# Kernel optimization log

Measured on AMD Instinct MI355X. Metric: run time of the kernel, lower is better.

Reference implementation:

```python
import jax, jax.numpy as jnp
import numpy as np

N = 177          # hardcoded in update(): view(1, 177, out_channels)
HEADS = 1
OUT = 128
EDGE_DIM = 1
NEG_SLOPE = 0.2
E = 500000


def _glorot(key, shape):
    stdv = np.sqrt(6.0 / (shape[-2] + shape[-1])).astype(np.float32)
    return jax.random.uniform(key, shape, jnp.float32, -stdv, stdv)


def setup_inputs() -> dict:
    key = jax.random.key(0)
    ks = jax.random.split(key, 6)
    x = jax.random.normal(ks[0], (1, N, 128), jnp.float32)
    edge_index = jax.random.randint(ks[1], (2, E), 0, N)
    edge_attr = jax.random.normal(ks[2], (E, EDGE_DIM), jnp.float32)
    weight = _glorot(ks[3], (128, HEADS * OUT))
    att = _glorot(ks[4], (1, HEADS, 2 * OUT + EDGE_DIM))
    edge_update1 = _glorot(ks[5], (OUT + EDGE_DIM, OUT))
    bias = jnp.zeros((OUT,), jnp.float32)
    return {"x": x, "edge_attr": edge_attr, "weight": weight, "att": att,
            "edge_update1": edge_update1, "bias": bias, "edge_index": edge_index}


def reference(x, edge_attr, weight, att, edge_update1, bias, edge_index):
    # node transform: [N, in] @ [in, H*C] -> [N, H, C]
    h = (x[0] @ weight).reshape(-1, HEADS, OUT)
    src, dst = edge_index[0], edge_index[1]   # PyG: row 0 = source (j), row 1 = target (i)
    x_j = h[src]                              # [E, H, C]
    x_i = h[dst]                              # [E, H, C]
    ea = jnp.broadcast_to(edge_attr[:, None, :], (edge_attr.shape[0], HEADS, EDGE_DIM))
    x_j = jnp.concatenate([x_j, ea], axis=-1)              # [E, H, C+edge_dim]
    # attention logits: sum over feature axis of cat([x_i, x_j]) * att
    alpha = (jnp.concatenate([x_i, x_j], axis=-1) * att).sum(axis=-1)  # [E, H]
    alpha = jax.nn.leaky_relu(alpha, NEG_SLOPE)
    # scatter softmax over target nodes (two-pass: segment max then segment sum)
    amax = jax.ops.segment_max(alpha, dst, num_segments=N)             # [N, H]
    e = jnp.exp(alpha - amax[dst])
    esum = jax.ops.segment_sum(e, dst, num_segments=N)                 # [N, H]
    alpha = e / (esum[dst] + 1e-16)
    # weighted messages, scatter-add aggregation
    msg = x_j * alpha[:, :, None]                                      # [E, H, C+edge_dim]
    aggr = jax.ops.segment_sum(msg, dst, num_segments=N)               # [N, H, C+edge_dim]
    out = aggr.mean(axis=1) @ edge_update1 + bias                      # [N, C]
    return out.reshape(1, N, OUT)
```

## Files before the change

### kernel.cpp

```cpp
#include <hip/hip_runtime.h>

#define NN 177
#define NEG 0.2f
#define QR 45
#define ROWP 180
#define QSLOTS_P (QR * ROWP)
#define SL 8192
#define NCHUNK 64
#define EBLOCKS (NCHUNK * 4)
#define ETH 512

#define AIP_OFF  0
#define AJP_OFF  384
#define H_OFF    768
#define PART_OFF 23424

__device__ __forceinline__ float4 f4add(float4 a, float4 b) {
    return make_float4(a.x + b.x, a.y + b.y, a.z + b.z, a.w + b.w);
}

__global__ __launch_bounds__(256)
void k_nodeH(const float* __restrict__ x, const float* __restrict__ w,
             const float* __restrict__ att, float* __restrict__ ws) {
    const int n = blockIdx.x, half = blockIdx.y;
    const int tid = threadIdx.x;
    const int j = tid & 63, kq = tid >> 6;
    __shared__ float xl[128];
    __shared__ float ph[256];
    if (tid < 128) xl[tid] = x[n * 128 + tid];
    __syncthreads();
    const float* wp = w + (size_t)(kq * 32) * 128 + half * 64 + j;
    float acc = 0.f;
#pragma unroll 8
    for (int k = 0; k < 32; ++k) acc += xl[kq * 32 + k] * wp[(size_t)k * 128];
    ph[tid] = acc;
    __syncthreads();
    if (tid < 64) {
        float hv = ph[j] + ph[64 + j] + ph[128 + j] + ph[192 + j];
        ws[H_OFF + n * 128 + half * 64 + j] = hv;
        float pa = hv * att[half * 64 + j];
        float pb = hv * att[128 + half * 64 + j];
#pragma unroll
        for (int m = 1; m < 64; m <<= 1) {
            pa += __shfl_xor(pa, m);
            pb += __shfl_xor(pb, m);
        }
        if (j == 0) {
            ws[AIP_OFF + 2 * n + half] = pa;
            ws[AJP_OFF + 2 * n + half] = pb;
        }
    }
}

__global__ __launch_bounds__(ETH, 8)
void k_edge(const int* __restrict__ ei, const float* __restrict__ ea,
            const float* __restrict__ att, float* __restrict__ ws, int E, int CH) {
    const int chunk = blockIdx.x & (NCHUNK - 1), q = blockIdx.x >> 6;
    const int dlo = q * QR;
    int drows = NN - dlo; if (drows > QR) drows = QR;
    __shared__ __align__(16) float Wl[QSLOTS_P];
    __shared__ float ajl[NN], ailq[QR], Mq[QR], llast[QR], mred[64];
    int tid = threadIdx.x;
    const float4 z4 = make_float4(0.f, 0.f, 0.f, 0.f);
    for (int i = tid; i < QSLOTS_P / 4; i += ETH) ((float4*)Wl)[i] = z4;
    for (int i = tid; i < NN; i += ETH)
        ajl[i] = ws[AJP_OFF + 2 * i] + ws[AJP_OFF + 2 * i + 1];
    if (tid < QR) llast[tid] = 0.f;
    __syncthreads();
    if (tid < 64) {
        float m = -1e30f;
        for (int i = tid; i < NN; i += 64) m = fmaxf(m, ajl[i]);
        mred[tid] = m;
    }
    __syncthreads();
    if (tid < 16) mred[tid] = fmaxf(fmaxf(mred[tid], mred[tid + 16]),
                                    fmaxf(mred[tid + 32], mred[tid + 48]));
    __syncthreads();
    if (tid < 4) mred[tid] = fmaxf(fmaxf(mred[tid], mred[tid + 4]),
                                   fmaxf(mred[tid + 8], mred[tid + 12]));
    __syncthreads();
    if (tid == 0) mred[0] = fmaxf(fmaxf(mred[0], mred[1]), fmaxf(mred[2], mred[3]));
    __syncthreads();
    const float ajmax = mred[0];
    if (tid < drows) {
        float a = ws[AIP_OFF + 2 * (dlo + tid)] + ws[AIP_OFF + 2 * (dlo + tid) + 1];
        ailq[tid] = a;
        float M = a + ajmax + 1.0f;
        Mq[tid] = (M > 0.f) ? M : NEG * M;
    }
    const float cc = att[2 * 128];
    __syncthreads();

    const int base = chunk * CH;
    int lim = base + CH; if (lim > E) lim = E;
    const bool aligned4 = ((E & 3) == 0);
    for (int e0 = base + tid * 4; e0 < lim; e0 += ETH * 4) {
        int4 sv, dv; float4 eav;
        if (aligned4 && e0 + 3 < lim) {
            sv  = *(const int4*)(ei + e0);
            dv  = *(const int4*)(ei + E + e0);
            eav = *(const float4*)(ea + e0);
        } else {
            int e1 = lim - e0;
            sv.x = (e1 > 0) ? ei[e0]     : 0; dv.x = (e1 > 0) ? ei[E + e0]     : -1; eav.x = (e1 > 0) ? ea[e0]     : 0.f;
            sv.y = (e1 > 1) ? ei[e0 + 1] : 0; dv.y = (e1 > 1) ? ei[E + e0 + 1] : -1; eav.y = (e1 > 1) ? ea[e0 + 1] : 0.f;
            sv.z = (e1 > 2) ? ei[e0 + 2] : 0; dv.z = (e1 > 2) ? ei[E + e0 + 2] : -1; eav.z = (e1 > 2) ? ea[e0 + 2] : 0.f;
            sv.w = (e1 > 3) ? ei[e0 + 3] : 0; dv.w = (e1 > 3) ? ei[E + e0 + 3] : -1; eav.w = (e1 > 3) ? ea[e0 + 3] : 0.f;
        }
#define PROC(SS, DD, EE) do {                                   \
            int d_ = (DD) - dlo;                                \
            if ((unsigned)d_ < (unsigned)drows) {               \
                float t_ = ailq[d_] + ajl[SS] + cc * (EE);      \
                t_ = (t_ > 0.f) ? t_ : NEG * t_;                \
                float ev_ = __expf(t_ - Mq[d_]);                \
                atomicAdd(&Wl[d_ * ROWP + (SS)], ev_);          \
                atomicAdd(&llast[d_], ev_ * (EE));              \
            }                                                   \
        } while (0)
        PROC(sv.x, dv.x, eav.x);
        PROC(sv.y, dv.y, eav.y);
        PROC(sv.z, dv.z, eav.z);
        PROC(sv.w, dv.w, eav.w);
#undef PROC
    }
    __syncthreads();
    float* part = ws + PART_OFF + (size_t)blockIdx.x * SL;
    for (int i = tid; i < QSLOTS_P / 4; i += ETH)
        ((float4*)part)[i] = ((const float4*)Wl)[i];
    if (tid < QR) part[QSLOTS_P + tid] = llast[tid];
}

__global__ __launch_bounds__(ETH)
void k_outC(const float* __restrict__ ws, const float* __restrict__ eu,
            const float* __restrict__ bias, float* __restrict__ out) {
    __shared__ __align__(16) float wl[ROWP];
    __shared__ float vl[128];
    __shared__ float red[128];
    __shared__ float sc[2];
    __shared__ __align__(16) float hl[89 * 128];
    __shared__ __align__(16) float pd[2048];
    const int n = blockIdx.x, tid = threadIdx.x;
    const int q = n / QR, r = n % QR;
    const size_t qbase = PART_OFF + (size_t)q * NCHUNK * SL;

    {
        const int lane = tid & 63, cg = tid >> 6;
        const int s4 = lane * 4;
        float4 acc = make_float4(0.f, 0.f, 0.f, 0.f);
        if (s4 < ROWP) {
            const float* p = ws + qbase + (size_t)(cg * 8) * SL + (size_t)r * ROWP + s4;
#pragma unroll
            for (int ch = 0; ch < 8; ++ch)
                acc = f4add(acc, *(const float4*)(p + (size_t)ch * SL));
        }
        ((float4*)pd)[tid] = acc;
    }
    if (tid < 64) red[tid] = ws[qbase + (size_t)tid * SL + QSLOTS_P + r];
    __syncthreads();
    if (tid < 256) ((float4*)pd)[tid] = f4add(((float4*)pd)[tid], ((float4*)pd)[tid + 256]);
    if (tid < 32) red[tid] += red[tid + 32];
    __syncthreads();
    if (tid < 128) ((float4*)pd)[tid] = f4add(((float4*)pd)[tid], ((float4*)pd)[tid + 128]);
    if (tid < 16) red[tid] += red[tid + 16];
    __syncthreads();
    if (tid < 64) {
        float4 v = f4add(((float4*)pd)[tid], ((float4*)pd)[tid + 64]);
        if (tid * 4 < ROWP) ((float4*)wl)[tid] = v;
    }
    if (tid < 8) red[tid] += red[tid + 8];
    __syncthreads();
    if (tid == 0) {
        float wv = 0.f;
#pragma unroll
        for (int i = 0; i < 8; ++i) wv += red[i];
        sc[0] = wv;
    }
    __syncthreads();
    if (tid < 128) red[tid] = wl[tid] + ((tid + 128 < NN) ? wl[tid + 128] : 0.f);
    __syncthreads();
    for (int off = 64; off > 0; off >>= 1) {
        if (tid < off) red[tid] += red[tid + off];
        __syncthreads();
    }
    if (tid == 0) sc[1] = red[0];

    const int c = tid & 127, g = tid >> 7;
    float vacc = 0.f;
    __syncthreads();
    for (int i = tid; i < 89 * 32; i += ETH)
        ((float4*)hl)[i] = ((const float4*)(ws + H_OFF))[i];
    __syncthreads();
    {
        int s0 = (g * 89) >> 2, s1 = ((g + 1) * 89) >> 2;
        for (int s = s0; s < s1; ++s) vacc += wl[s] * hl[s * 128 + c];
    }
    __syncthreads();
    for (int i = tid; i < 88 * 32; i += ETH)
        ((float4*)hl)[i] = ((const float4*)(ws + H_OFF + 89 * 128))[i];
    __syncthreads();
    {
        int s0 = (g * 88) >> 2, s1 = ((g + 1) * 88) >> 2;
        for (int s = s0; s < s1; ++s) vacc += wl[89 + s] * hl[s * 128 + c];
    }
    pd[tid] = vacc;
    __syncthreads();
    if (tid < 128) vl[tid] = (pd[tid] + pd[128 + tid]) + (pd[256 + tid] + pd[384 + tid]);
    __syncthreads();

    {
        const int kg = tid >> 7;
        float oacc = 0.f;
        const float* ep = eu + (size_t)(kg * 32) * 128 + c;
#pragma unroll 8
        for (int k = 0; k < 32; ++k) oacc += vl[kg * 32 + k] * ep[(size_t)k * 128];
        pd[tid] = oacc;
    }
    __syncthreads();
    if (tid < 128) {
        float dot = (pd[tid] + pd[128 + tid]) + (pd[256 + tid] + pd[384 + tid]);
        out[n * 128 + tid] = (dot + sc[0] * eu[128 * 128 + tid]) / (sc[1] + 1e-16f) + bias[tid];
    }
}

extern "C" void kernel_launch(void* const* d_in, const int* in_sizes, int n_in,
                              void* d_out, int out_size, void* d_ws, size_t ws_size,
                              hipStream_t stream) {
    const float* x     = (const float*)d_in[0];
    const float* eattr = (const float*)d_in[1];
    const float* w     = (const float*)d_in[2];
    const float* att   = (const float*)d_in[3];
    const float* eu    = (const float*)d_in[4];
    const float* bias  = (const float*)d_in[5];
    const int*   ei    = (const int*)d_in[6];
    int E = in_sizes[6] / 2;
    int CH = (((E + NCHUNK - 1) / NCHUNK) + 3) & ~3;
    float* ws = (float*)d_ws;

    k_nodeH<<<dim3(NN, 2), 256, 0, stream>>>(x, w, att, ws);
    k_edge<<<EBLOCKS, ETH, 0, stream>>>(ei, eattr, att, ws, E, CH);
    k_outC<<<NN, ETH, 0, stream>>>(ws, eu, bias, (float*)d_out);
}
```

Baseline: 32.39 us.

## Fuse node transform into edge kernel via algebraic attention-vector precompute

Removes the separate node-transform kernel launch. Each edge block now computes u=W·att_i and v=W·att_j, then evaluates per-node attention logits as x·u and x·v redundantly for all nodes. The first 177 blocks also compute and store the full h rows needed by the output kernel. This saves a launch and the inter-kernel dependency, at the cost of redundant per-block prologue work (reading W and x in every block) and a slightly different floating-point summation order.

```diff
diff --git a/kernel.cpp b/kernel.cpp
--- a/kernel.cpp
+++ b/kernel.cpp
@@ -10,8 +10,6 @@
 #define EBLOCKS (NCHUNK * 4)
 #define ETH 512
 
-#define AIP_OFF  0
-#define AJP_OFF  384
 #define H_OFF    768
 #define PART_OFF 23424
 
@@ -19,54 +17,52 @@
     return make_float4(a.x + b.x, a.y + b.y, a.z + b.z, a.w + b.w);
 }
 
-__global__ __launch_bounds__(256)
-void k_nodeH(const float* __restrict__ x, const float* __restrict__ w,
-             const float* __restrict__ att, float* __restrict__ ws) {
-    const int n = blockIdx.x, half = blockIdx.y;
+__global__ __launch_bounds__(ETH)
+void k_edgeA(const float* __restrict__ x, const float* __restrict__ ea,
+             const float* __restrict__ w, const float* __restrict__ att,
+             const int* __restrict__ ei, float* __restrict__ ws, int E, int CH) {
+    __shared__ __align__(16) float Wl[QSLOTS_P];
+    __shared__ float ajl[NN], ail[NN], Mq[QR], llast[QR], mred[64];
+    __shared__ float uvec[128], vvec[128], atl[257], xl[128];
     const int tid = threadIdx.x;
-    const int j = tid & 63, kq = tid >> 6;
-    __shared__ float xl[128];
-    __shared__ float ph[256];
-    if (tid < 128) xl[tid] = x[n * 128 + tid];
-    __syncthreads();
-    const float* wp = w + (size_t)(kq * 32) * 128 + half * 64 + j;
-    float acc = 0.f;
-#pragma unroll 8
-    for (int k = 0; k < 32; ++k) acc += xl[kq * 32 + k] * wp[(size_t)k * 128];
-    ph[tid] = acc;
-    __syncthreads();
-    if (tid < 64) {
-        float hv = ph[j] + ph[64 + j] + ph[128 + j] + ph[192 + j];
-        ws[H_OFF + n * 128 + half * 64 + j] = hv;
-        float pa = hv * att[half * 64 + j];
-        float pb = hv * att[128 + half * 64 + j];
-#pragma unroll
-        for (int m = 1; m < 64; m <<= 1) {
-            pa += __shfl_xor(pa, m);
-            pb += __shfl_xor(pb, m);
-        }
-        if (j == 0) {
-            ws[AIP_OFF + 2 * n + half] = pa;
-            ws[AJP_OFF + 2 * n + half] = pb;
-        }
-    }
-}
-
-__global__ __launch_bounds__(ETH, 8)
-void k_edge(const int* __restrict__ ei, const float* __restrict__ ea,
-            const float* __restrict__ att, float* __restrict__ ws, int E, int CH) {
-    const int chunk = blockIdx.x & (NCHUNK - 1), q = blockIdx.x >> 6;
+    const int bid = blockIdx.x;
+    const int chunk = bid & (NCHUNK - 1), q = bid >> 6;
     const int dlo = q * QR;
     int drows = NN - dlo; if (drows > QR) drows = QR;
-    __shared__ __align__(16) float Wl[QSLOTS_P];
-    __shared__ float ajl[NN], ailq[QR], Mq[QR], llast[QR], mred[64];
-    int tid = threadIdx.x;
-    const float4 z4 = make_float4(0.f, 0.f, 0.f, 0.f);
-    for (int i = tid; i < QSLOTS_P / 4; i += ETH) ((float4*)Wl)[i] = z4;
-    for (int i = tid; i < NN; i += ETH)
-        ajl[i] = ws[AJP_OFF + 2 * i] + ws[AJP_OFF + 2 * i + 1];
-    if (tid < QR) llast[tid] = 0.f;
-    __syncthreads();
+
+    for (int i = tid; i < 257; i += ETH) atl[i] = att[i];
+    if (bid < NN && tid < 128) xl[tid] = x[bid * 128 + tid];
+    __syncthreads();
+
+    const float4* w4 = (const float4*)w;
+#pragma unroll
+    for (int i = 0; i < 8; ++i) {
+        int f = i * 512 + tid;
+        int k = f >> 5, c4 = (f & 31) << 2;
+        float4 wv = w4[f];
+        float pu = wv.x*atl[c4]     + wv.y*atl[c4+1]     + wv.z*atl[c4+2]     + wv.w*atl[c4+3];
+        float pv = wv.x*atl[128+c4] + wv.y*atl[128+c4+1] + wv.z*atl[128+c4+2] + wv.w*atl[128+c4+3];
+#pragma unroll
+        for (int m = 1; m <= 16; m <<= 1) { pu += __shfl_xor(pu, m); pv += __shfl_xor(pv, m); }
+        if ((tid & 31) == 0) { uvec[k] = pu; vvec[k] = pv; }
+    }
+    __syncthreads();
+
+    const float4* x4p = (const float4*)x;
+#pragma unroll
+    for (int i = 0; i < 12; ++i) {
+        int f = i * 512 + tid;
+        bool valid = f < NN * 32;
+        float4 xv = valid ? x4p[f] : make_float4(0.f, 0.f, 0.f, 0.f);
+        int c4 = (f & 31) << 2;
+        float pa = xv.x*uvec[c4] + xv.y*uvec[c4+1] + xv.z*uvec[c4+2] + xv.w*uvec[c4+3];
+        float pb = xv.x*vvec[c4] + xv.y*vvec[c4+1] + xv.z*vvec[c4+2] + xv.w*vvec[c4+3];
+#pragma unroll
+        for (int m = 1; m <= 16; m <<= 1) { pa += __shfl_xor(pa, m); pb += __shfl_xor(pb, m); }
+        if (valid && (tid & 31) == 0) { int n = f >> 5; ail[n] = pa; ajl[n] = pb; }
+    }
+    __syncthreads();
+
     if (tid < 64) {
         float m = -1e30f;
         for (int i = tid; i < NN; i += 64) m = fmaxf(m, ajl[i]);
@@ -82,13 +78,28 @@
     if (tid == 0) mred[0] = fmaxf(fmaxf(mred[0], mred[1]), fmaxf(mred[2], mred[3]));
     __syncthreads();
     const float ajmax = mred[0];
+
+    if (bid < NN) {
+        const int c = tid & 127, kq = tid >> 7;
+        const float* wp = w + (size_t)(kq * 32) * 128 + c;
+        float a = 0.f;
+#pragma unroll 8
+        for (int k = 0; k < 32; ++k) a += xl[kq * 32 + k] * wp[(size_t)k * 128];
+        Wl[tid] = a;
+        __syncthreads();
+        if (tid < 128)
+            ws[H_OFF + bid * 128 + tid] = (Wl[tid] + Wl[128 + tid]) + (Wl[256 + tid] + Wl[384 + tid]);
+        __syncthreads();
+    }
+
+    const float4 z4 = make_float4(0.f, 0.f, 0.f, 0.f);
+    for (int i = tid; i < QSLOTS_P / 4; i += ETH) ((float4*)Wl)[i] = z4;
+    if (tid < QR) llast[tid] = 0.f;
     if (tid < drows) {
-        float a = ws[AIP_OFF + 2 * (dlo + tid)] + ws[AIP_OFF + 2 * (dlo + tid) + 1];
-        ailq[tid] = a;
-        float M = a + ajmax + 1.0f;
+        float M = ail[dlo + tid] + ajmax + 1.0f;
         Mq[tid] = (M > 0.f) ? M : NEG * M;
     }
-    const float cc = att[2 * 128];
+    const float cc = atl[256];
     __syncthreads();
 
     const int base = chunk * CH;
@@ -110,7 +121,7 @@
 #define PROC(SS, DD, EE) do {                                   \
             int d_ = (DD) - dlo;                                \
             if ((unsigned)d_ < (unsigned)drows) {               \
-                float t_ = ailq[d_] + ajl[SS] + cc * (EE);      \
+                float t_ = ail[dlo + d_] + ajl[SS] + cc * (EE); \
                 t_ = (t_ > 0.f) ? t_ : NEG * t_;                \
                 float ev_ = __expf(t_ - Mq[d_]);                \
                 atomicAdd(&Wl[d_ * ROWP + (SS)], ev_);          \
@@ -124,7 +135,7 @@
 #undef PROC
     }
     __syncthreads();
-    float* part = ws + PART_OFF + (size_t)blockIdx.x * SL;
+    float* part = ws + PART_OFF + (size_t)bid * SL;
     for (int i = tid; i < QSLOTS_P / 4; i += ETH)
         ((float4*)part)[i] = ((const float4*)Wl)[i];
     if (tid < QR) part[QSLOTS_P + tid] = llast[tid];
@@ -236,7 +247,6 @@
     int CH = (((E + NCHUNK - 1) / NCHUNK) + 3) & ~3;
     float* ws = (float*)d_ws;
 
-    k_nodeH<<<dim3(NN, 2), 256, 0, stream>>>(x, w, att, ws);
-    k_edge<<<EBLOCKS, ETH, 0, stream>>>(ei, eattr, att, ws, E, CH);
+    k_edgeA<<<EBLOCKS, ETH, 0, stream>>>(x, eattr, w, att, ei, ws, E, CH);
     k_outC<<<NN, ETH, 0, stream>>>(ws, eu, bias, (float*)d_out);
 }
```

Measured after the change: 34.09 us. 1.05x slower.

## Reassociate aggregation to weight x before projection, dropping stored node features

Applied to the files above, without the earlier changes.

The node kernel no longer writes the projected features h to workspace. The output kernel instead forms the weighted sum of raw x rows and multiplies that single vector by the weight matrix, using (sum w_s x_s) W = sum w_s (x_s W). This removes the global write of h, the staging of about 88 KB of h per block into LDS, and the large shared-memory footprint. The cost is an extra 128x128 matvec per block, and x is read straight from global memory without LDS staging.

```diff
diff --git a/kernel.cpp b/kernel.cpp
--- a/kernel.cpp
+++ b/kernel.cpp
@@ -12,15 +12,14 @@
 
 #define AIP_OFF  0
 #define AJP_OFF  384
-#define H_OFF    768
-#define PART_OFF 23424
+#define PART_OFF 768
 
 __device__ __forceinline__ float4 f4add(float4 a, float4 b) {
     return make_float4(a.x + b.x, a.y + b.y, a.z + b.z, a.w + b.w);
 }
 
 __global__ __launch_bounds__(256)
-void k_nodeH(const float* __restrict__ x, const float* __restrict__ w,
+void k_nodeA(const float* __restrict__ x, const float* __restrict__ w,
              const float* __restrict__ att, float* __restrict__ ws) {
     const int n = blockIdx.x, half = blockIdx.y;
     const int tid = threadIdx.x;
@@ -37,7 +36,6 @@
     __syncthreads();
     if (tid < 64) {
         float hv = ph[j] + ph[64 + j] + ph[128 + j] + ph[192 + j];
-        ws[H_OFF + n * 128 + half * 64 + j] = hv;
         float pa = hv * att[half * 64 + j];
         float pb = hv * att[128 + half * 64 + j];
 #pragma unroll
@@ -131,13 +129,13 @@
 }
 
 __global__ __launch_bounds__(ETH)
-void k_outC(const float* __restrict__ ws, const float* __restrict__ eu,
+void k_outD(const float* __restrict__ ws, const float* __restrict__ x,
+            const float* __restrict__ w, const float* __restrict__ eu,
             const float* __restrict__ bias, float* __restrict__ out) {
     __shared__ __align__(16) float wl[ROWP];
-    __shared__ float vl[128];
     __shared__ float red[128];
     __shared__ float sc[2];
-    __shared__ __align__(16) float hl[89 * 128];
+    __shared__ float yl[128], vl[128];
     __shared__ __align__(16) float pd[2048];
     const int n = blockIdx.x, tid = threadIdx.x;
     const int q = n / QR, r = n % QR;
@@ -183,37 +181,37 @@
         __syncthreads();
     }
     if (tid == 0) sc[1] = red[0];
+    __syncthreads();
 
     const int c = tid & 127, g = tid >> 7;
-    float vacc = 0.f;
-    __syncthreads();
-    for (int i = tid; i < 89 * 32; i += ETH)
-        ((float4*)hl)[i] = ((const float4*)(ws + H_OFF))[i];
-    __syncthreads();
-    {
-        int s0 = (g * 89) >> 2, s1 = ((g + 1) * 89) >> 2;
-        for (int s = s0; s < s1; ++s) vacc += wl[s] * hl[s * 128 + c];
-    }
-    __syncthreads();
-    for (int i = tid; i < 88 * 32; i += ETH)
-        ((float4*)hl)[i] = ((const float4*)(ws + H_OFF + 89 * 128))[i];
-    __syncthreads();
-    {
-        int s0 = (g * 88) >> 2, s1 = ((g + 1) * 88) >> 2;
-        for (int s = s0; s < s1; ++s) vacc += wl[89 + s] * hl[s * 128 + c];
-    }
-    pd[tid] = vacc;
+
+    {
+        float acc = 0.f;
+        int s0 = g * 45, s1 = s0 + 45; if (s1 > NN) s1 = NN;
+        for (int s = s0; s < s1; ++s) acc += wl[s] * x[s * 128 + c];
+        pd[tid] = acc;
+    }
+    __syncthreads();
+    if (tid < 128) yl[tid] = (pd[tid] + pd[128 + tid]) + (pd[256 + tid] + pd[384 + tid]);
+    __syncthreads();
+
+    {
+        float acc = 0.f;
+        const float* wp = w + (size_t)(g * 32) * 128 + c;
+#pragma unroll 8
+        for (int k = 0; k < 32; ++k) acc += yl[g * 32 + k] * wp[(size_t)k * 128];
+        pd[tid] = acc;
+    }
     __syncthreads();
     if (tid < 128) vl[tid] = (pd[tid] + pd[128 + tid]) + (pd[256 + tid] + pd[384 + tid]);
     __syncthreads();
 
     {
-        const int kg = tid >> 7;
-        float oacc = 0.f;
-        const float* ep = eu + (size_t)(kg * 32) * 128 + c;
+        float acc = 0.f;
+        const float* ep = eu + (size_t)(g * 32) * 128 + c;
 #pragma unroll 8
-        for (int k = 0; k < 32; ++k) oacc += vl[kg * 32 + k] * ep[(size_t)k * 128];
-        pd[tid] = oacc;
+        for (int k = 0; k < 32; ++k) acc += vl[g * 32 + k] * ep[(size_t)k * 128];
+        pd[tid] = acc;
     }
     __syncthreads();
     if (tid < 128) {
@@ -236,7 +234,7 @@
     int CH = (((E + NCHUNK - 1) / NCHUNK) + 3) & ~3;
     float* ws = (float*)d_ws;
 
-    k_nodeH<<<dim3(NN, 2), 256, 0, stream>>>(x, w, att, ws);
+    k_nodeA<<<dim3(NN, 2), 256, 0, stream>>>(x, w, att, ws);
     k_edge<<<EBLOCKS, ETH, 0, stream>>>(ei, eattr, att, ws, E, CH);
-    k_outC<<<NN, ETH, 0, stream>>>(ws, eu, bias, (float*)d_out);
-}
+    k_outD<<<NN, ETH, 0, stream>>>(ws, x, w, eu, bias, (float*)d_out);
+}
```

Result: no change. 32.24 us (median of 2 runs) (-0.4%).
